# Kernel tuning notes

Hardware: AMD Instinct MI355X
Metric: run time of the kernel (lower is better)

The kernel has to match this reference:

```python
import jax, jax.numpy as jnp
import numpy as np

PH, PW = 7, 7          # output_size
GRID = 2               # sampling_ratio
SCALES = (0.25, 0.125, 0.0625, 0.03125)  # 2^round(log2(feat/img)) per level
LVL_MIN, LVL_MAX = 2, 5                  # -log2(scales[0]), -log2(scales[-1])
CANON_SCALE, CANON_LVL = 224.0, 4.0
EPS = 1e-6


def setup_inputs() -> dict:
    key = jax.random.key(0)
    ks = jax.random.split(key, 6)
    B, C = 2, 256
    sizes = [(200, 200), (100, 100), (50, 50), (25, 25)]
    inp = {f"feat{i}": jax.random.normal(ks[i], (B, C, h, w), jnp.float32)
           for i, (h, w) in enumerate(sizes)}
    Nb = 256
    # boxes in 800x800 image coords, x1y1 + positive wh so 0<=x1<x2, 0<=y1<y2
    xy = jax.random.uniform(ks[4], (B, Nb, 2), jnp.float32, 0.0, 700.0)
    wh = jax.random.uniform(ks[5], (B, Nb, 2), jnp.float32, 32.0, 512.0)
    inp["boxes"] = jnp.concatenate([xy, xy + wh], axis=-1)
    return inp


def _roi_align_level(feat, b_idx, rois, scale):
    """torchvision roi_align, aligned=False. feat [B,C,H,W], rois [R,4] -> [R,C,PH,PW]."""
    H, W = feat.shape[2], feat.shape[3]
    x1 = rois[:, 0] * scale
    y1 = rois[:, 1] * scale
    x2 = rois[:, 2] * scale
    y2 = rois[:, 3] * scale
    roi_w = jnp.maximum(x2 - x1, 1.0)
    roi_h = jnp.maximum(y2 - y1, 1.0)
    bin_w = roi_w / PW
    bin_h = roi_h / PH
    # sub-bin sampling offsets: (bin + (i+0.5)/grid) for each bin, flattened [PH*GRID]
    gy = (jnp.arange(PH, dtype=jnp.float32)[:, None]
          + (jnp.arange(GRID, dtype=jnp.float32)[None, :] + 0.5) / GRID).reshape(-1)
    gx = (jnp.arange(PW, dtype=jnp.float32)[:, None]
          + (jnp.arange(GRID, dtype=jnp.float32)[None, :] + 0.5) / GRID).reshape(-1)
    ys = y1[:, None] + gy[None, :] * bin_h[:, None]   # [R, PH*G]
    xs = x1[:, None] + gx[None, :] * bin_w[:, None]   # [R, PW*G]
    y = ys[:, :, None]                                 # [R, PH*G, 1]
    x = xs[:, None, :]                                 # [R, 1, PW*G]
    valid = (y >= -1.0) & (y <= H) & (x >= -1.0) & (x <= W)
    yc = jnp.clip(y, 0.0, H - 1)
    xc = jnp.clip(x, 0.0, W - 1)
    yl = jnp.floor(yc).astype(jnp.int32)
    xl = jnp.floor(xc).astype(jnp.int32)
    yh = jnp.minimum(yl + 1, H - 1)
    xh = jnp.minimum(xl + 1, W - 1)
    ly = yc - yl.astype(yc.dtype)
    lx = xc - xl.astype(xc.dtype)
    hy = 1.0 - ly
    hx = 1.0 - lx
    b = b_idx[:, None, None]

    def gather(yi, xi):
        # advanced indexing with slice in channel dim -> [R, PH*G, PW*G, C]
        return feat[b, :, yi, xi]

    val = ((hy * hx)[..., None] * gather(yl, xl)
           + (hy * lx)[..., None] * gather(yl, xh)
           + (ly * hx)[..., None] * gather(yh, xl)
           + (ly * lx)[..., None] * gather(yh, xh))
    val = jnp.where(valid[..., None], val, 0.0)
    R, C = rois.shape[0], feat.shape[1]
    # average over the GRIDxGRID sampling points of each bin
    val = val.reshape(R, PH, GRID, PW, GRID, C).mean(axis=(2, 4))  # [R,PH,PW,C]
    return jnp.transpose(val, (0, 3, 1, 2))                        # [R,C,PH,PW]


def reference(feat0, feat1, feat2, feat3, boxes):
    feats = [feat0, feat1, feat2, feat3]
    B, Nb = boxes.shape[0], boxes.shape[1]
    rois = boxes.reshape(-1, 4)                               # convert_to_roi_format
    b_idx = jnp.repeat(jnp.arange(B), Nb)
    # LevelMapper (FPN eq. 1)
    s = jnp.sqrt(jnp.maximum((rois[:, 2] - rois[:, 0]) * (rois[:, 3] - rois[:, 1]), 0.0))
    lvl = jnp.floor(CANON_LVL + jnp.log2(s / CANON_SCALE + EPS))
    lvl = jnp.clip(lvl, LVL_MIN, LVL_MAX).astype(jnp.int32) - LVL_MIN  # [R] in [0,3]
    out = jnp.zeros((rois.shape[0], feats[0].shape[1], PH, PW), feats[0].dtype)
    for l, (f, sc) in enumerate(zip(feats, SCALES)):
        pooled = _roi_align_level(f, b_idx, rois, sc)
        out = jnp.where((lvl == l)[:, None, None, None], pooled, out)
    return out
```

## Files before the change

kernel.cpp:

```cpp
#include <hip/hip_runtime.h>


#define PHW 49
#define NCHUNK 8
#define CH 32
#define PSIZE 1024

__global__ __launch_bounds__(256) void msroi_kernel(
    const float* __restrict__ f0, const float* __restrict__ f1,
    const float* __restrict__ f2, const float* __restrict__ f3,
    const float* __restrict__ boxes, float* __restrict__ out)
{
    const int C = 256, Nb = 256;
    const int r = blockIdx.x;
    const int chunk = blockIdx.y;
    const int tid = threadIdx.x;
    const int b = r / Nb;

    const int bin = tid >> 2;
    const int q   = tid & 3;
    const bool active = bin < PHW;

    const float x1b = boxes[r * 4 + 0];
    const float y1b = boxes[r * 4 + 1];
    const float x2b = boxes[r * 4 + 2];
    const float y2b = boxes[r * 4 + 3];
    const float area = fmaxf((x2b - x1b) * (y2b - y1b), 0.0f);
    const float s = sqrtf(area);
    float lv = floorf(4.0f + log2f(s / 224.0f + 1e-6f));
    lv = fminf(fmaxf(lv, 2.0f), 5.0f);
    const int lvl = (int)lv - 2;

    const float* feat;
    int H, W;
    float scale;
    switch (lvl) {
        case 0:  feat = f0; H = 200; W = 200; scale = 0.25f;    break;
        case 1:  feat = f1; H = 100; W = 100; scale = 0.125f;   break;
        case 2:  feat = f2; H = 50;  W = 50;  scale = 0.0625f;  break;
        default: feat = f3; H = 25;  W = 25;  scale = 0.03125f; break;
    }
    const int HW = H * W;

    const float x1 = x1b * scale, y1 = y1b * scale;
    const float x2 = x2b * scale, y2 = y2b * scale;
    const float roi_w = fmaxf(x2 - x1, 1.0f);
    const float roi_h = fmaxf(y2 - y1, 1.0f);
    const float bin_w = roi_w * (1.0f / 7.0f);
    const float bin_h = roi_h * (1.0f / 7.0f);

    const float ys0 = fminf(fmaxf(y1 + 0.25f * bin_h, 0.0f), (float)(H - 1));
    const float ys1 = fminf(fmaxf(y1 + 6.75f * bin_h, 0.0f), (float)(H - 1));
    const float xs0 = fminf(fmaxf(x1 + 0.25f * bin_w, 0.0f), (float)(W - 1));
    const float xs1 = fminf(fmaxf(x1 + 6.75f * bin_w, 0.0f), (float)(W - 1));
    const int row0 = (int)floorf(ys0);
    const int row1 = min((int)floorf(ys1) + 1, H - 1);
    const int col0 = (int)floorf(xs0);
    const int col1 = min((int)floorf(xs1) + 1, W - 1);
    const int prows = row1 - row0 + 1;
    const int pcols = col1 - col0 + 1;
    const int psize = prows * pcols;
    const int wstride = W - pcols;
    const float inv_pcols = 1.0f / (float)pcols;

    int goff[4];
#pragma unroll
    for (int k = 0; k < 4; ++k) {
        const int e = tid + k * 256;
        const int ec = min(e, psize - 1);
        const int rr = (int)floorf(((float)ec + 0.5f) * inv_pcols);
        goff[k] = ec + rr * wstride;
    }
    const int kmax = (psize + 255) >> 8;

    int   offs[4];
    float wts[4];
    {
        const int bb = active ? bin : 0;
        const int ph = bb / 7;
        const int pw = bb - ph * 7;
        const int iy = q >> 1, ix = q & 1;
        const float gy = (float)ph + ((float)iy + 0.5f) * 0.5f;
        const float gx = (float)pw + ((float)ix + 0.5f) * 0.5f;
        const float y = y1 + gy * bin_h;
        const float x = x1 + gx * bin_w;
        const bool valid = (y >= -1.0f) && (y <= (float)H) &&
                           (x >= -1.0f) && (x <= (float)W);
        const float yc = fminf(fmaxf(y, 0.0f), (float)(H - 1));
        const float xc = fminf(fmaxf(x, 0.0f), (float)(W - 1));
        const int yl = (int)floorf(yc);
        const int xl = (int)floorf(xc);
        const int yh = min(yl + 1, H - 1);
        const int xh = min(xl + 1, W - 1);
        const float ly = yc - (float)yl;
        const float lx = xc - (float)xl;
        const float hy = 1.0f - ly, hx = 1.0f - lx;
        const float m = valid ? 0.25f : 0.0f;
        const int ry0 = (yl - row0) * pcols, ry1 = (yh - row0) * pcols;
        const int cx0 = xl - col0, cx1 = xh - col0;
        offs[0] = ry0 + cx0;  wts[0] = hy * hx * m;
        offs[1] = ry0 + cx1;  wts[1] = hy * lx * m;
        offs[2] = ry1 + cx0;  wts[2] = ly * hx * m;
        offs[3] = ry1 + cx1;  wts[3] = ly * lx * m;
    }

    __shared__ float4 lds4[PSIZE];

    const int cbase = chunk * CH;
    const float* __restrict__ fch =
        feat + (size_t)(b * C + cbase) * HW + (row0 * W + col0);
    float* __restrict__ outp =
        out + (size_t)r * C * PHW + (size_t)cbase * PHW;

    float4 buf[4];

#define LOADR(CCV)                                                         \
    do {                                                                   \
        const float* __restrict__ g0 = fch + (size_t)((CCV) + 0) * HW;     \
        const float* __restrict__ g1 = fch + (size_t)((CCV) + 1) * HW;     \
        const float* __restrict__ g2 = fch + (size_t)((CCV) + 2) * HW;     \
        const float* __restrict__ g3 = fch + (size_t)((CCV) + 3) * HW;     \
        _Pragma("unroll")                                                  \
        for (int k = 0; k < 4; ++k) {                                      \
            if (k < kmax) {       \
                buf[k].x = g0[goff[k]];                                    \
                buf[k].y = g1[goff[k]];                                    \
                buf[k].z = g2[goff[k]];                                    \
                buf[k].w = g3[goff[k]];                                    \
            }                                                              \
        }                                                                  \
    } while (0)

    LOADR(0);
    for (int cc = 0; cc < CH; cc += 4) {
        __syncthreads();
#pragma unroll
        for (int k = 0; k < 4; ++k)
            if (k < kmax) lds4[tid + k * 256] = buf[k];
        __syncthreads();

        if (cc + 4 < CH) LOADR(cc + 4);

        if (active) {
            float4 a = make_float4(0.0f, 0.0f, 0.0f, 0.0f);
#pragma unroll
            for (int j = 0; j < 4; ++j) {
                const float4 v = lds4[offs[j]];
                a.x += wts[j] * v.x;
                a.y += wts[j] * v.y;
                a.z += wts[j] * v.z;
                a.w += wts[j] * v.w;
            }
            a.x += __shfl_xor(a.x, 1); a.y += __shfl_xor(a.y, 1);
            a.z += __shfl_xor(a.z, 1); a.w += __shfl_xor(a.w, 1);
            a.x += __shfl_xor(a.x, 2); a.y += __shfl_xor(a.y, 2);
            a.z += __shfl_xor(a.z, 2); a.w += __shfl_xor(a.w, 2);
            const float vout = (q == 0) ? a.x : (q == 1) ? a.y
                             : (q == 2) ? a.z : a.w;
            outp[(size_t)(cc + q) * PHW + bin] = vout;
        }
    }
#undef LOADR
}

extern "C" void kernel_launch(void* const* d_in, const int* in_sizes, int n_in,
                              void* d_out, int out_size, void* d_ws, size_t ws_size,
                              hipStream_t stream) {
    const float* f0 = (const float*)d_in[0];
    const float* f1 = (const float*)d_in[1];
    const float* f2 = (const float*)d_in[2];
    const float* f3 = (const float*)d_in[3];
    const float* boxes = (const float*)d_in[4];
    float* out = (float*)d_out;

    const int R = in_sizes[4] / 4;
    dim3 grid(R, NCHUNK);
    msroi_kernel<<<grid, 256, 0, stream>>>(f0, f1, f2, f3, boxes, out);
}
```

Measured before the change: 180.8 us.

## Double-buffer global loads and use barriers that skip vmcnt waits

Adds a second register buffer so loads for two channel groups ahead are in flight while the current group is written to LDS and consumed. Replaces __syncthreads with a custom barrier that waits only on LDS counters, so outstanding global loads need not drain at each barrier. This aims to hide global-memory latency behind compute, at the cost of more registers. It also relies on the compiler inserting the correct vmcnt waits before the buffered values are used.

```diff
diff --git a/kernel.cpp b/kernel.cpp
--- a/kernel.cpp
+++ b/kernel.cpp
@@ -5,6 +5,12 @@
 #define NCHUNK 8
 #define CH 32
 #define PSIZE 1024
+
+#define BARRIER_KEEP_VMCNT()                                   \
+    do {                                                       \
+        asm volatile("s_waitcnt lgkmcnt(0)" ::: "memory");     \
+        __builtin_amdgcn_s_barrier();                          \
+    } while (0)
 
 __global__ __launch_bounds__(256) void msroi_kernel(
     const float* __restrict__ f0, const float* __restrict__ f1,
@@ -112,9 +118,9 @@
     float* __restrict__ outp =
         out + (size_t)r * C * PHW + (size_t)cbase * PHW;
 
-    float4 buf[4];
-
-#define LOADR(CCV)                                                         \
+    float4 bufA[4], bufB[4];
+
+#define LOADR(BUF, CCV)                                                    \
     do {                                                                   \
         const float* __restrict__ g0 = fch + (size_t)((CCV) + 0) * HW;     \
         const float* __restrict__ g1 = fch + (size_t)((CCV) + 1) * HW;     \
@@ -123,44 +129,63 @@
         _Pragma("unroll")                                                  \
         for (int k = 0; k < 4; ++k) {                                      \
             if (k < kmax) {       \
-                buf[k].x = g0[goff[k]];                                    \
-                buf[k].y = g1[goff[k]];                                    \
-                buf[k].z = g2[goff[k]];                                    \
-                buf[k].w = g3[goff[k]];                                    \
+                BUF[k].x = g0[goff[k]];                                    \
+                BUF[k].y = g1[goff[k]];                                    \
+                BUF[k].z = g2[goff[k]];                                    \
+                BUF[k].w = g3[goff[k]];                                    \
             }                                                              \
         }                                                                  \
     } while (0)
 
-    LOADR(0);
-    for (int cc = 0; cc < CH; cc += 4) {
-        __syncthreads();
+#define WRITELDS(BUF)                                                      \
+    do {                                                                   \
+        _Pragma("unroll")                                                  \
+        for (int k = 0; k < 4; ++k)                                        \
+            if (k < kmax) lds4[tid + k * 256] = BUF[k];                    \
+    } while (0)
+
+#define COMPUTE(CCV)                                                       \
+    do {                                                                   \
+        if (active) {                                                      \
+            float4 a = make_float4(0.0f, 0.0f, 0.0f, 0.0f);                \
+            _Pragma("unroll")                                              \
+            for (int j = 0; j < 4; ++j) {                                  \
+                const float4 v = lds4[offs[j]];                            \
+                a.x += wts[j] * v.x;                                       \
+                a.y += wts[j] * v.y;                                       \
+                a.z += wts[j] * v.z;                                       \
+                a.w += wts[j] * v.w;                                       \
+            }                                                              \
+            a.x += __shfl_xor(a.x, 1); a.y += __shfl_xor(a.y, 1);          \
+            a.z += __shfl_xor(a.z, 1); a.w += __shfl_xor(a.w, 1);          \
+            a.x += __shfl_xor(a.x, 2); a.y += __shfl_xor(a.y, 2);          \
+            a.z += __shfl_xor(a.z, 2); a.w += __shfl_xor(a.w, 2);          \
+            const float vout = (q == 0) ? a.x : (q == 1) ? a.y             \
+                             : (q == 2) ? a.z : a.w;                       \
+            outp[(size_t)((CCV) + q) * PHW + bin] = vout;                  \
+        }                                                                  \
+    } while (0)
+
+    LOADR(bufA, 0);
+    LOADR(bufB, 4);
+
 #pragma unroll
-        for (int k = 0; k < 4; ++k)
-            if (k < kmax) lds4[tid + k * 256] = buf[k];
-        __syncthreads();
-
-        if (cc + 4 < CH) LOADR(cc + 4);
-
-        if (active) {
-            float4 a = make_float4(0.0f, 0.0f, 0.0f, 0.0f);
-#pragma unroll
-            for (int j = 0; j < 4; ++j) {
-                const float4 v = lds4[offs[j]];
-                a.x += wts[j] * v.x;
-                a.y += wts[j] * v.y;
-                a.z += wts[j] * v.z;
-                a.w += wts[j] * v.w;
-            }
-            a.x += __shfl_xor(a.x, 1); a.y += __shfl_xor(a.y, 1);
-            a.z += __shfl_xor(a.z, 1); a.w += __shfl_xor(a.w, 1);
-            a.x += __shfl_xor(a.x, 2); a.y += __shfl_xor(a.y, 2);
-            a.z += __shfl_xor(a.z, 2); a.w += __shfl_xor(a.w, 2);
-            const float vout = (q == 0) ? a.x : (q == 1) ? a.y
-                             : (q == 2) ? a.z : a.w;
-            outp[(size_t)(cc + q) * PHW + bin] = vout;
-        }
+    for (int c = 0; c < CH; c += 8) {
+        BARRIER_KEEP_VMCNT();
+        WRITELDS(bufA);
+        if (c + 8 < CH) LOADR(bufA, c + 8);
+        BARRIER_KEEP_VMCNT();
+        COMPUTE(c);
+
+        BARRIER_KEEP_VMCNT();
+        WRITELDS(bufB);
+        if (c + 12 < CH) LOADR(bufB, c + 12);
+        BARRIER_KEEP_VMCNT();
+        COMPUTE(c + 4);
     }
 #undef LOADR
+#undef WRITELDS
+#undef COMPUTE
 }
 
 extern "C" void kernel_launch(void* const* d_in, const int* in_sizes, int n_in,
```

Measured after the change: 183.4 us. About the same (+1.4%).
